# Optimization experiments

Measured on AMD Instinct MI355X. Metric: run time of the kernel, lower is better.

## Reference

```python
import jax, jax.numpy as jnp
import numpy as np

B, T, C, H = 2, 2048, 1024, 16
Dh = C // H  # 64
EPS = 1e-5


def layer_norm(x, g, b):
    mu = jnp.mean(x, axis=-1, keepdims=True)
    var = jnp.mean(jnp.square(x - mu), axis=-1, keepdims=True)
    return (x - mu) * jax.lax.rsqrt(var + EPS) * g + b


def setup_inputs() -> dict:
    key = jax.random.key(0)
    ks = jax.random.split(key, 12)
    s = 0.02
    return {
        "x": jax.random.normal(ks[0], (B, T, C), dtype=jnp.float32),
        # per-head projections, stacked: (H, C, Dh), no bias (bias=False in source)
        "Wq": jax.random.normal(ks[1], (H, C, Dh), dtype=jnp.float32) * s,
        "Wk": jax.random.normal(ks[2], (H, C, Dh), dtype=jnp.float32) * s,
        "Wv": jax.random.normal(ks[3], (H, C, Dh), dtype=jnp.float32) * s,
        "Wo": jax.random.normal(ks[4], (H * Dh, C), dtype=jnp.float32) * s,
        "bo": jnp.zeros((C,), dtype=jnp.float32),
        "W1": jax.random.normal(ks[5], (C, 4 * C), dtype=jnp.float32) * s,
        "b1": jnp.zeros((4 * C,), dtype=jnp.float32),
        "W2": jax.random.normal(ks[6], (4 * C, C), dtype=jnp.float32) * s,
        "b2": jnp.zeros((C,), dtype=jnp.float32),
        "g1": jnp.ones((C,), dtype=jnp.float32),
        "be1": jnp.zeros((C,), dtype=jnp.float32),
        "g2": jnp.ones((C,), dtype=jnp.float32),
        "be2": jnp.zeros((C,), dtype=jnp.float32),
    }


def reference(x, Wq, Wk, Wv, Wo, bo, W1, b1, W2, b2, g1, be1, g2, be2):
    # --- self-attention sublayer ---
    h = layer_norm(x, g1, be1)                       # (B,T,C)
    q = jnp.einsum("btc,hcd->bhtd", h, Wq)
    k = jnp.einsum("btc,hcd->bhtd", h, Wk)
    v = jnp.einsum("btc,hcd->bhtd", h, Wv)
    # NOTE: source scales by C**-0.5 (head INPUT dim), not head_size**-0.5
    scores = jnp.einsum("bhqd,bhkd->bhqk", q, k) * (C ** -0.5)
    # encoder=True default => mask is all ones => no masking applied
    w = jax.nn.softmax(scores, axis=-1)              # (B,H,T,T)
    o = jnp.einsum("bhqk,bhkd->bhqd", w, v)          # (B,H,T,Dh)
    o = o.transpose(0, 2, 1, 3).reshape(B, T, H * Dh)  # concat heads
    attn = o @ Wo + bo                               # output projection
    x = x + attn
    # --- feed-forward sublayer ---
    h2 = layer_norm(x, g2, be2)
    ff = jax.nn.relu(h2 @ W1 + b1) @ W2 + b2
    return x + ff
```

## Files before the change

### kernel.cpp

```cpp
#include <hip/hip_runtime.h>
#include <hip/hip_bf16.h>

#define BT   4096
#define CD   1024
#define TD   2048
#define NH   16
#define DH   64
#define BB   2

typedef __attribute__((ext_vector_type(8))) short bf16x8;
typedef __attribute__((ext_vector_type(4))) short bf16x4;
typedef __attribute__((ext_vector_type(4))) float f32x4;
typedef __attribute__((ext_vector_type(2))) unsigned int u32x2;

__device__ inline short f2bf(float f) {
    union { float fv; unsigned u; } x; x.fv = f;
    unsigned r = x.u + 0x7fffu + ((x.u >> 16) & 1u);
    return (short)(r >> 16);
}
__device__ inline float bf2f(short s) {
    union { unsigned u; float f; } x; x.u = ((unsigned)(unsigned short)s) << 16;
    return x.f;
}
__device__ inline unsigned pk2bf(float a, float b) {
    union { __hip_bfloat162 h; unsigned u; } cv;
    cv.h = __float22bfloat162_rn(float2{a, b});
    return cv.u;
}

#if __has_builtin(__builtin_amdgcn_exp2f)
#define EXP2(x) __builtin_amdgcn_exp2f(x)
#else
#define EXP2(x) exp2f(x)
#endif

#if __has_builtin(__builtin_amdgcn_mfma_f32_16x16x16bf16_1k)
#define MFMA16x16(a, b, c) __builtin_amdgcn_mfma_f32_16x16x16bf16_1k(a, b, c, 0, 0, 0)
#elif __has_builtin(__builtin_amdgcn_mfma_f32_16x16x16_bf16)
#define MFMA16x16(a, b, c) __builtin_amdgcn_mfma_f32_16x16x16_bf16(a, b, c, 0, 0, 0)
#else
__device__ inline f32x4 mfma16_asm(bf16x4 a, bf16x4 b, f32x4 c) {
    f32x4 d;
    asm volatile("v_mfma_f32_16x16x16_bf16 %0, %1, %2, %3"
                 : "=v"(d) : "v"(a), "v"(b), "v"(c));
    return d;
}
#define MFMA16x16(a, b, c) mfma16_asm(a, b, c)
#endif

__device__ inline void gload_lds16(const short* g, short* lds) {
    __builtin_amdgcn_global_load_lds(
        (const __attribute__((address_space(1))) void*)g,
        (__attribute__((address_space(3))) void*)lds, 16, 0, 0);
}

__launch_bounds__(256)
__global__ void ln_kernel(const float* __restrict__ x,
                          const float* __restrict__ g,
                          const float* __restrict__ be,
                          short* __restrict__ out) {
    __shared__ float red[2][4];
    const int row = blockIdx.x;
    const float* xr = x + (size_t)row * CD;
    float s = 0.f, ss = 0.f;
    for (int c = threadIdx.x; c < CD; c += 256) {
        float v = xr[c];
        s += v; ss += v * v;
    }
    #pragma unroll
    for (int off = 32; off > 0; off >>= 1) {
        s  += __shfl_down(s,  off, 64);
        ss += __shfl_down(ss, off, 64);
    }
    int wid = threadIdx.x >> 6, lane = threadIdx.x & 63;
    if (lane == 0) { red[0][wid] = s; red[1][wid] = ss; }
    __syncthreads();
    float sum   = red[0][0] + red[0][1] + red[0][2] + red[0][3];
    float sumsq = red[1][0] + red[1][1] + red[1][2] + red[1][3];
    float mu   = sum * (1.f / CD);
    float var  = sumsq * (1.f / CD) - mu * mu;
    float rstd = rsqrtf(var + 1e-5f);
    short* orow = out + (size_t)row * CD;
    for (int c = threadIdx.x; c < CD; c += 256) {
        float v = xr[c];
        orow[c] = f2bf((v - mu) * rstd * g[c] + be[c]);
    }
}

__launch_bounds__(256)
__global__ void prep_weights(const float* __restrict__ Wq, const float* __restrict__ Wk,
                             const float* __restrict__ Wv, const float* __restrict__ Wo,
                             const float* __restrict__ W1, const float* __restrict__ W2,
                             short* __restrict__ wqt, short* __restrict__ wot,
                             short* __restrict__ w1t, short* __restrict__ w2t) {
    __shared__ float tt[64][65];
    const int id = blockIdx.x;
    const float* in; short* out; int R, Cc, r0, c0;
    if (id < 768) {
        int which = id >> 8, rem = id & 255, hh = rem >> 4, ry = rem & 15;
        in  = (which == 0 ? Wq : which == 1 ? Wk : Wv) + (size_t)hh * CD * DH;
        out = wqt + (size_t)which * CD * CD + (size_t)hh * DH * CD;
        R = CD; Cc = DH; r0 = ry * 64; c0 = 0;
    } else if (id < 1024) {
        int t = id - 768;  in = Wo; out = wot; R = CD;     Cc = CD;     r0 = (t >> 4) * 64; c0 = (t & 15) * 64;
    } else if (id < 2048) {
        int t = id - 1024; in = W1; out = w1t; R = CD;     Cc = 4 * CD; r0 = (t >> 6) * 64; c0 = (t & 63) * 64;
    } else {
        int t = id - 2048; in = W2; out = w2t; R = 4 * CD; Cc = CD;     r0 = (t >> 4) * 64; c0 = (t & 15) * 64;
    }
    const int tid = threadIdx.x;
    #pragma unroll
    for (int i = 0; i < 16; ++i) {
        int e = i * 256 + tid;
        tt[e >> 6][e & 63] = in[(size_t)(r0 + (e >> 6)) * Cc + c0 + (e & 63)];
    }
    __syncthreads();
    #pragma unroll
    for (int i = 0; i < 16; ++i) {
        int e = i * 256 + tid;
        out[(size_t)(c0 + (e >> 6)) * R + r0 + (e & 63)] = f2bf(tt[e & 63][e >> 6]);
    }
}

__launch_bounds__(256)
__global__ void vtrans(const short* __restrict__ vin, short* __restrict__ vout) {
    __shared__ short t[64 * 65];
    const int tid = threadIdx.x;
    const int bh = blockIdx.y;
    const int t0 = blockIdx.x * 64;
    const int b = bh >> 4, h = bh & 15;
    const short* src = vin + (size_t)b * TD * CD + (size_t)h * DH;
    short* dst = vout + (size_t)bh * DH * TD;
    #pragma unroll
    for (int i = 0; i < 16; ++i) {
        int e = i * 256 + tid;
        t[(e >> 6) * 65 + (e & 63)] = src[(size_t)(t0 + (e >> 6)) * CD + (e & 63)];
    }
    __syncthreads();
    #pragma unroll
    for (int i = 0; i < 16; ++i) {
        int e = i * 256 + tid;
        int d = e >> 6, tt = e & 63;
        dst[(size_t)d * TD + t0 + tt] = t[tt * 65 + d];
    }
}

template <int MODE, int TN>
__launch_bounds__(256)
__global__ void gemm_mfma(const short* __restrict__ A,
                          const short* __restrict__ Bt,
                          const float* __restrict__ bias,
                          const float* __restrict__ resid,
                          float* __restrict__ outf,
                          short* __restrict__ outb,
                          int N, int K) {
    __shared__ short As[3][128 * 32];
    __shared__ short Bs[3][TN * 32];
    const int tid = threadIdx.x;
    const int w = tid >> 6, lane = tid & 63;
    const int quad = lane >> 4, l16 = lane & 15;
    const int wr = w >> 1, wc = w & 1;
    const int m0 = blockIdx.y * 128, n0 = blockIdx.x * TN;
    const int NT = TN / 32;

    f32x4 acc[4][NT] = {};

    auto STAGE = [&](int kt, int bi) {
        const int k0 = kt * 32;
        #pragma unroll
        for (int i = 0; i < 2; ++i) {
            int s = i * 256 + tid;
            int row = s >> 2, kc = (s & 3) ^ ((row >> 1) & 3);
            gload_lds16(A + (size_t)(m0 + row) * K + k0 + kc * 8,
                        &As[bi][(i * 256 + w * 64) * 8]);
        }
        #pragma unroll
        for (int i = 0; i < TN / 64; ++i) {
            int s = i * 256 + tid;
            int row = s >> 2, kc = (s & 3) ^ ((row >> 1) & 3);
            gload_lds16(Bt + (size_t)(n0 + row) * K + k0 + kc * 8,
                        &Bs[bi][(i * 256 + w * 64) * 8]);
        }
    };

    auto COMPUTE = [&](int bi) {
        const int xo = (quad ^ ((l16 >> 1) & 3)) * 8;
        bf16x8 a[4], b[NT];
        #pragma unroll
        for (int mt = 0; mt < 4; ++mt)
            a[mt] = *(const bf16x8*)&As[bi][(wr * 64 + mt * 16 + l16) * 32 + xo];
        #pragma unroll
        for (int nt = 0; nt < NT; ++nt)
            b[nt] = *(const bf16x8*)&Bs[bi][(wc * (TN / 2) + nt * 16 + l16) * 32 + xo];
        #pragma unroll
        for (int mt = 0; mt < 4; ++mt)
            #pragma unroll
            for (int nt = 0; nt < NT; ++nt)
                acc[mt][nt] = __builtin_amdgcn_mfma_f32_16x16x32_bf16(a[mt], b[nt], acc[mt][nt], 0, 0, 0);
    };

    const int nk = K >> 5;
    STAGE(0, 0);
    STAGE(1, 1);
    int bi = 0;
    for (int t = 0; t < nk - 1; ++t) {
        if (TN == 128) asm volatile("s_waitcnt vmcnt(4)" ::: "memory");
        else           asm volatile("s_waitcnt vmcnt(3)" ::: "memory");
        __builtin_amdgcn_s_barrier();
        asm volatile("" ::: "memory");
        int bn = bi + 2 >= 3 ? bi - 1 : bi + 2;
        if (t + 2 < nk) STAGE(t + 2, bn);
        COMPUTE(bi);
        bi = bi + 1 >= 3 ? 0 : bi + 1;
    }
    asm volatile("s_waitcnt vmcnt(0)" ::: "memory");
    __builtin_amdgcn_s_barrier();
    asm volatile("" ::: "memory");
    COMPUTE(bi);

    const float qsc = (MODE == 5 && n0 < CD) ? 0.03125f * 1.44269504f : 1.0f;
    short* ob5 = (MODE == 5) ? outb + (size_t)(n0 >> 10) * BT * CD : nullptr;

    #pragma unroll
    for (int mt = 0; mt < 4; ++mt)
        #pragma unroll
        for (int nt = 0; nt < NT; ++nt)
            #pragma unroll
            for (int reg = 0; reg < 4; ++reg) {
                int row = m0 + wr * 64 + mt * 16 + quad * 4 + reg;
                int col = n0 + wc * (TN / 2) + nt * 16 + l16;
                float v = acc[mt][nt][reg];
                if (MODE == 1) { v += bias[col] + resid[(size_t)row * N + col];
                                 outf[(size_t)row * N + col] = v; }
                if (MODE == 2) { v = fmaxf(v + bias[col], 0.f);
                                 outb[(size_t)row * N + col] = f2bf(v); }
                if (MODE == 5) { ob5[(size_t)row * CD + (col & 1023)] = f2bf(v * qsc); }
            }
}

#define BQ   128
#define BK   64
#define STR  68

__launch_bounds__(256)
__global__ void attn_mfma(const short* __restrict__ q,
                          const short* __restrict__ k,
                          const short* __restrict__ vt,
                          short* __restrict__ opart,
                          float* __restrict__ lpart) {
    __shared__ short Ks[2][BK * STR];
    __shared__ short Vt[2][DH * STR];

    const int tid  = threadIdx.x;
    const int w = tid >> 6, lane = tid & 63;
    const int quad = lane >> 4, l16 = lane & 15;
    const int h = blockIdx.y;
    const int b = blockIdx.z >> 1, split = blockIdx.z & 1;
    const int q0 = blockIdx.x * BQ;
    const size_t base  = (size_t)b * TD * CD + (size_t)h * DH;
    const size_t vbase = (size_t)(b * NH + h) * DH * TD;

    bf16x8 qf[2][2];
    #pragma unroll
    for (int rt = 0; rt < 2; ++rt) {
        const short* qp = q + base + (size_t)(q0 + w * 32 + rt * 16 + l16) * CD;
        qf[rt][0] = *(const bf16x8*)&qp[quad * 8];
        qf[rt][1] = *(const bf16x8*)&qp[32 + quad * 8];
    }

    float l_p[2] = {};
    f32x4 O[2][4] = {};

    const int kbeg = split * (TD / 2);
    const int NTI = (TD / 2) / BK;

    const int r8 = tid >> 3, c8 = (tid & 7) * 8;
    const short* kg = k + base + c8;
    const short* vg = vt + vbase + (size_t)r8 * TD + c8;

#define ISSUE_T(t, K0, K1, V0, V1) do {                                   \
        const size_t ko_ = (size_t)(kbeg + (t) * BK);                     \
        K0 = *(const bf16x8*)&kg[(ko_ + r8) * CD];                        \
        K1 = *(const bf16x8*)&kg[(ko_ + r8 + 32) * CD];                   \
        V0 = *(const bf16x8*)&vg[ko_];                                    \
        V1 = *(const bf16x8*)&vg[(size_t)32 * TD + ko_];                  \
    } while (0)

#define WRITE_T(buf, K0, K1, V0, V1) do {                                 \
        *(bf16x8*)&Ks[buf][r8 * STR + c8] = K0;                           \
        *(bf16x8*)&Ks[buf][(r8 + 32) * STR + c8] = K1;                    \
        *(bf16x8*)&Vt[buf][r8 * STR + c8] = V0;                           \
        *(bf16x8*)&Vt[buf][(r8 + 32) * STR + c8] = V1;                    \
    } while (0)

#define COMPUTE_T(buf) do {                                               \
        __builtin_amdgcn_s_setprio(1);                                    \
        _Pragma("unroll")                                                 \
        for (int ct = 0; ct < 4; ++ct) {                                  \
            bf16x8 kb0 = *(const bf16x8*)&Ks[buf][(ct * 16 + l16) * STR + quad * 8]; \
            bf16x8 kb1 = *(const bf16x8*)&Ks[buf][(ct * 16 + l16) * STR + 32 + quad * 8]; \
            bf16x4 pa[2];                                                 \
            _Pragma("unroll")                                             \
            for (int rt = 0; rt < 2; ++rt) {                              \
                f32x4 acc = (f32x4){0.f, 0.f, 0.f, 0.f};                  \
                acc = __builtin_amdgcn_mfma_f32_16x16x32_bf16(kb0, qf[rt][0], acc, 0, 0, 0); \
                acc = __builtin_amdgcn_mfma_f32_16x16x32_bf16(kb1, qf[rt][1], acc, 0, 0, 0); \
                float p0 = EXP2(acc[0]), p1 = EXP2(acc[1]);               \
                float p2 = EXP2(acc[2]), p3 = EXP2(acc[3]);               \
                l_p[rt] += (p0 + p1) + (p2 + p3);                         \
                union { u32x2 u; bf16x4 s; } cv_;                         \
                cv_.u = (u32x2){pk2bf(p0, p1), pk2bf(p2, p3)};            \
                pa[rt] = cv_.s;                                           \
            }                                                             \
            _Pragma("unroll")                                             \
            for (int dt = 0; dt < 4; ++dt) {                              \
                bf16x4 vb = *(const bf16x4*)&Vt[buf][(dt * 16 + l16) * STR + ct * 16 + quad * 4]; \
                O[0][dt] = MFMA16x16(pa[0], vb, O[0][dt]);                \
                O[1][dt] = MFMA16x16(pa[1], vb, O[1][dt]);                \
            }                                                             \
        }                                                                 \
        __builtin_amdgcn_s_setprio(0);                                    \
    } while (0)

    bf16x8 kA0, kA1, vA0, vA1;
    bf16x8 kB0, kB1, vB0, vB1;

    ISSUE_T(0, kA0, kA1, vA0, vA1);
    WRITE_T(0, kA0, kA1, vA0, vA1);
    ISSUE_T(1, kA0, kA1, vA0, vA1);
    __syncthreads();

    for (int it = 0; it < NTI; it += 2) {
        if (it + 2 < NTI) ISSUE_T(it + 2, kB0, kB1, vB0, vB1);
        COMPUTE_T(0);
        WRITE_T(1, kA0, kA1, vA0, vA1);
        __syncthreads();
        if (it + 3 < NTI) ISSUE_T(it + 3, kA0, kA1, vA0, vA1);
        COMPUTE_T(1);
        if (it + 2 < NTI) WRITE_T(0, kB0, kB1, vB0, vB1);
        __syncthreads();
    }
#undef ISSUE_T
#undef WRITE_T
#undef COMPUTE_T

    short* osp = opart + (size_t)split * BT * CD;
    float* lsp = lpart + (size_t)split * BB * NH * TD + (size_t)(b * NH + h) * TD;
    #pragma unroll
    for (int rt = 0; rt < 2; ++rt) {
        float l = l_p[rt];
        l += __shfl_xor(l, 16, 64);
        l += __shfl_xor(l, 32, 64);
        if (lane < 16) lsp[q0 + w * 32 + rt * 16 + lane] = l;
        #pragma unroll
        for (int reg = 0; reg < 4; ++reg) {
            int row = q0 + w * 32 + rt * 16 + quad * 4 + reg;
            short* op = osp + base + (size_t)row * CD;
            #pragma unroll
            for (int dt = 0; dt < 4; ++dt)
                op[dt * 16 + l16] = f2bf(O[rt][dt][reg]);
        }
    }
}

__launch_bounds__(256)
__global__ void attn_combine(const short* __restrict__ opart,
                             const float* __restrict__ lpart,
                             short* __restrict__ ob) {
    const size_t idx = ((size_t)blockIdx.x * 256 + threadIdx.x) * 8;
    const int row = (int)(idx >> 10);
    const int col = (int)(idx & 1023);
    const int b = row >> 11, qq = row & (TD - 1), hh = col >> 6;
    const size_t lbase = (size_t)(b * NH + hh) * TD + qq;
    const float l0 = lpart[lbase];
    const float l1 = lpart[(size_t)BB * NH * TD + lbase];
    const float inv = 1.f / (l0 + l1);
    bf16x8 a = *(const bf16x8*)&opart[idx];
    bf16x8 c = *(const bf16x8*)&opart[(size_t)BT * CD + idx];
    bf16x8 r;
    #pragma unroll
    for (int j = 0; j < 8; ++j)
        r[j] = f2bf((bf2f(a[j]) + bf2f(c[j])) * inv);
    *(bf16x8*)&ob[idx] = r;
}

extern "C" void kernel_launch(void* const* d_in, const int* in_sizes, int n_in,
                              void* d_out, int out_size, void* d_ws, size_t ws_size,
                              hipStream_t stream) {
    const float* x   = (const float*)d_in[0];
    const float* Wq  = (const float*)d_in[1];
    const float* Wk  = (const float*)d_in[2];
    const float* Wv  = (const float*)d_in[3];
    const float* Wo  = (const float*)d_in[4];
    const float* bo  = (const float*)d_in[5];
    const float* W1  = (const float*)d_in[6];
    const float* b1  = (const float*)d_in[7];
    const float* W2  = (const float*)d_in[8];
    const float* b2  = (const float*)d_in[9];
    const float* g1  = (const float*)d_in[10];
    const float* be1 = (const float*)d_in[11];
    const float* g2  = (const float*)d_in[12];
    const float* be2 = (const float*)d_in[13];
    float* out = (float*)d_out;

    const size_t SZ = (size_t)BT * CD;
    float* ws  = (float*)d_ws;
    short* qbf = (short*)ws;
    short* kbf = qbf + SZ;
    short* vbf = qbf + 2 * SZ;
    float* lpart = ws + SZ + SZ / 2;
    short* opart = (short*)(ws + 2 * SZ);
    float* x1  = ws + 2 * SZ;
    short* h   = (short*)(ws + 3 * SZ);
    short* ob  = (short*)(ws + 3 * SZ + SZ / 2);
    short* wqt = (short*)(ws + 4 * SZ);
    short* wot = wqt + 3 * CD * CD;
    short* w1t = (short*)(ws + 4 * SZ + SZ / 2);
    short* w2t = (short*)(ws + 5 * SZ);
    short* vtg = (short*)(ws + 5 * SZ + SZ / 2);
    short* ff1 = (short*)ws;

    ln_kernel<<<BT, 256, 0, stream>>>(x, g1, be1, h);

    prep_weights<<<3072, 256, 0, stream>>>(Wq, Wk, Wv, Wo, W1, W2, wqt, wot, w1t, w2t);

    gemm_mfma<5, 128><<<dim3(24, 32), 256, 0, stream>>>(h, wqt, nullptr, nullptr, nullptr, qbf, 3 * CD, CD);

    vtrans<<<dim3(TD / 64, 2 * NH), 256, 0, stream>>>(vbf, vtg);

    attn_mfma<<<dim3(TD / BQ, NH, BB * 2), 256, 0, stream>>>(qbf, kbf, vtg, opart, lpart);

    attn_combine<<<dim3((int)(SZ / (256 * 8))), 256, 0, stream>>>(opart, lpart, ob);

    gemm_mfma<1, 128><<<dim3(8, 32), 256, 0, stream>>>(ob, wot, bo, x, x1, nullptr, CD, CD);

    ln_kernel<<<BT, 256, 0, stream>>>(x1, g2, be2, h);

    gemm_mfma<2, 128><<<dim3(32, 32), 256, 0, stream>>>(h, w1t, b1, nullptr, nullptr, ff1, 4 * CD, CD);

    gemm_mfma<1, 128><<<dim3(8, 32), 256, 0, stream>>>(ff1, w2t, b2, x1, out, nullptr, CD, 4 * CD);
}
```

Baseline: 381.0 us.

## Split K across two warp groups in N=1024 GEMMs with LDS reduction

Adds a GR template parameter so the output-projection and FFN2 GEMMs (only 256 blocks each) run 512 threads per block. Each 256-thread half processes half of K with its own triple-buffered LDS, and the partial accumulators are then summed through shared memory before the epilogue. This targets low occupancy and long K loops on the narrow GEMMs. In exchange it doubles LDS use per block and adds a reduction step with extra barriers.

```diff
diff --git a/kernel.cpp b/kernel.cpp
--- a/kernel.cpp
+++ b/kernel.cpp
@@ -145,8 +145,8 @@
     }
 }
 
-template <int MODE, int TN>
-__launch_bounds__(256)
+template <int MODE, int TN, int GR>
+__launch_bounds__(GR * 256)
 __global__ void gemm_mfma(const short* __restrict__ A,
                           const short* __restrict__ Bt,
                           const float* __restrict__ bias,
@@ -154,44 +154,54 @@
                           float* __restrict__ outf,
                           short* __restrict__ outb,
                           int N, int K) {
-    __shared__ short As[3][128 * 32];
-    __shared__ short Bs[3][TN * 32];
+    __shared__ __align__(16) short smem[GR * 3 * (128 + TN) * 32];
     const int tid = threadIdx.x;
-    const int w = tid >> 6, lane = tid & 63;
+    const int kgrp = (GR == 2) ? (tid >> 8) : 0;
+    const int tid256 = tid & 255;
+    const int w4 = tid256 >> 6, lane = tid & 63;
     const int quad = lane >> 4, l16 = lane & 15;
-    const int wr = w >> 1, wc = w & 1;
+    const int wr = w4 >> 1, wc = w4 & 1;
     const int m0 = blockIdx.y * 128, n0 = blockIdx.x * TN;
     const int NT = TN / 32;
+    const int kbase = kgrp * (K / GR);
+
+    short* grpBase = smem + (size_t)kgrp * 3 * (128 + TN) * 32;
+#define AS(bi) (grpBase + (bi) * (128 + TN) * 32)
+#define BS(bi) (AS(bi) + 128 * 32)
 
     f32x4 acc[4][NT] = {};
 
     auto STAGE = [&](int kt, int bi) {
-        const int k0 = kt * 32;
+        const int k0 = kbase + kt * 32;
+        short* as = AS(bi);
+        short* bs = BS(bi);
         #pragma unroll
         for (int i = 0; i < 2; ++i) {
-            int s = i * 256 + tid;
+            int s = i * 256 + tid256;
             int row = s >> 2, kc = (s & 3) ^ ((row >> 1) & 3);
             gload_lds16(A + (size_t)(m0 + row) * K + k0 + kc * 8,
-                        &As[bi][(i * 256 + w * 64) * 8]);
+                        &as[(i * 256 + w4 * 64) * 8]);
         }
         #pragma unroll
         for (int i = 0; i < TN / 64; ++i) {
-            int s = i * 256 + tid;
+            int s = i * 256 + tid256;
             int row = s >> 2, kc = (s & 3) ^ ((row >> 1) & 3);
             gload_lds16(Bt + (size_t)(n0 + row) * K + k0 + kc * 8,
-                        &Bs[bi][(i * 256 + w * 64) * 8]);
+                        &bs[(i * 256 + w4 * 64) * 8]);
         }
     };
 
     auto COMPUTE = [&](int bi) {
         const int xo = (quad ^ ((l16 >> 1) & 3)) * 8;
+        const short* as = AS(bi);
+        const short* bs = BS(bi);
         bf16x8 a[4], b[NT];
         #pragma unroll
         for (int mt = 0; mt < 4; ++mt)
-            a[mt] = *(const bf16x8*)&As[bi][(wr * 64 + mt * 16 + l16) * 32 + xo];
+            a[mt] = *(const bf16x8*)&as[(wr * 64 + mt * 16 + l16) * 32 + xo];
         #pragma unroll
         for (int nt = 0; nt < NT; ++nt)
-            b[nt] = *(const bf16x8*)&Bs[bi][(wc * (TN / 2) + nt * 16 + l16) * 32 + xo];
+            b[nt] = *(const bf16x8*)&bs[(wc * (TN / 2) + nt * 16 + l16) * 32 + xo];
         #pragma unroll
         for (int mt = 0; mt < 4; ++mt)
             #pragma unroll
@@ -199,13 +209,12 @@
                 acc[mt][nt] = __builtin_amdgcn_mfma_f32_16x16x32_bf16(a[mt], b[nt], acc[mt][nt], 0, 0, 0);
     };
 
-    const int nk = K >> 5;
+    const int nk = (K / GR) >> 5;
     STAGE(0, 0);
     STAGE(1, 1);
     int bi = 0;
     for (int t = 0; t < nk - 1; ++t) {
-        if (TN == 128) asm volatile("s_waitcnt vmcnt(4)" ::: "memory");
-        else           asm volatile("s_waitcnt vmcnt(3)" ::: "memory");
+        asm volatile("s_waitcnt vmcnt(4)" ::: "memory");
         __builtin_amdgcn_s_barrier();
         asm volatile("" ::: "memory");
         int bn = bi + 2 >= 3 ? bi - 1 : bi + 2;
@@ -217,6 +226,27 @@
     __builtin_amdgcn_s_barrier();
     asm volatile("" ::: "memory");
     COMPUTE(bi);
+
+    if (GR == 2) {
+        float* red = (float*)smem;
+        __syncthreads();
+        if (kgrp == 1) {
+            #pragma unroll
+            for (int mt = 0; mt < 4; ++mt)
+                #pragma unroll
+                for (int nt = 0; nt < NT; ++nt)
+                    *(f32x4*)&red[((mt * NT + nt) * 256 + w4 * 64 + lane) * 4] = acc[mt][nt];
+        }
+        __syncthreads();
+        if (kgrp == 1) return;
+        #pragma unroll
+        for (int mt = 0; mt < 4; ++mt)
+            #pragma unroll
+            for (int nt = 0; nt < NT; ++nt) {
+                f32x4 p = *(const f32x4*)&red[((mt * NT + nt) * 256 + w4 * 64 + lane) * 4];
+                acc[mt][nt] += p;
+            }
+    }
 
     const float qsc = (MODE == 5 && n0 < CD) ? 0.03125f * 1.44269504f : 1.0f;
     short* ob5 = (MODE == 5) ? outb + (size_t)(n0 >> 10) * BT * CD : nullptr;
@@ -236,6 +266,8 @@
                                  outb[(size_t)row * N + col] = f2bf(v); }
                 if (MODE == 5) { ob5[(size_t)row * CD + (col & 1023)] = f2bf(v * qsc); }
             }
+#undef AS
+#undef BS
 }
 
 #define BQ   128
@@ -424,7 +456,7 @@
 
     prep_weights<<<3072, 256, 0, stream>>>(Wq, Wk, Wv, Wo, W1, W2, wqt, wot, w1t, w2t);
 
-    gemm_mfma<5, 128><<<dim3(24, 32), 256, 0, stream>>>(h, wqt, nullptr, nullptr, nullptr, qbf, 3 * CD, CD);
+    gemm_mfma<5, 128, 1><<<dim3(24, 32), 256, 0, stream>>>(h, wqt, nullptr, nullptr, nullptr, qbf, 3 * CD, CD);
 
     vtrans<<<dim3(TD / 64, 2 * NH), 256, 0, stream>>>(vbf, vtg);
 
@@ -432,11 +464,11 @@
 
     attn_combine<<<dim3((int)(SZ / (256 * 8))), 256, 0, stream>>>(opart, lpart, ob);
 
-    gemm_mfma<1, 128><<<dim3(8, 32), 256, 0, stream>>>(ob, wot, bo, x, x1, nullptr, CD, CD);
+    gemm_mfma<1, 128, 2><<<dim3(8, 32), 512, 0, stream>>>(ob, wot, bo, x, x1, nullptr, CD, CD);
 
     ln_kernel<<<BT, 256, 0, stream>>>(x1, g2, be2, h);
 
-    gemm_mfma<2, 128><<<dim3(32, 32), 256, 0, stream>>>(h, w1t, b1, nullptr, nullptr, ff1, 4 * CD, CD);
-
-    gemm_mfma<1, 128><<<dim3(8, 32), 256, 0, stream>>>(ff1, w2t, b2, x1, out, nullptr, CD, 4 * CD);
-}
+    gemm_mfma<2, 128, 1><<<dim3(32, 32), 256, 0, stream>>>(h, w1t, b1, nullptr, nullptr, ff1, 4 * CD, CD);
+
+    gemm_mfma<1, 128, 2><<<dim3(8, 32), 512, 0, stream>>>(ff1, w2t, b2, x1, out, nullptr, CD, 4 * CD);
+}
```

Result: faster. 340.9 us (-10.5%).
